# Performance work log

Measured on AMD Instinct MI355X. Metric: run time of the kernel, lower is better.

## Reference

```python
import jax, jax.numpy as jnp
import numpy as np

EPS = 1e-5


def _bn(x, g, b):
    # BatchNorm1d in training mode: batch mean, biased variance, eps=1e-5
    m = jnp.mean(x, axis=0)
    v = jnp.var(x, axis=0)
    return (x - m) * jax.lax.rsqrt(v + EPS) * g + b


def setup_inputs() -> dict:
    key = jax.random.key(0)
    ks = jax.random.split(key, 16)
    B, N, F, H = 4096, 128, 4, 32
    w = lambda k, o, i: jax.random.normal(k, (o, i), jnp.float32) * 0.3
    d = {
        'u': jax.random.normal(ks[0], (B, N, F), jnp.float32),
        'mask': jnp.ones((B * N, 1), jnp.int32),
        # MLPphi params
        'p_bn1_g': jnp.ones((F,), jnp.float32), 'p_bn1_b': jnp.zeros((F,), jnp.float32), 'p_w1': w(ks[1], H, F),
        'p_bn2_g': jnp.ones((H,), jnp.float32), 'p_bn2_b': jnp.zeros((H,), jnp.float32), 'p_w2': w(ks[2], H, H),
        'p_bn3_g': jnp.ones((H,), jnp.float32), 'p_bn3_b': jnp.zeros((H,), jnp.float32), 'p_w3': w(ks[3], H, H),
        # MLPomega params
        'o_bn1_g': jnp.ones((F,), jnp.float32), 'o_bn1_b': jnp.zeros((F,), jnp.float32), 'o_w1': w(ks[4], H, F),
        'o_bn2_g': jnp.ones((H,), jnp.float32), 'o_bn2_b': jnp.zeros((H,), jnp.float32), 'o_w2': w(ks[5], H, H),
        'o_bn3_g': jnp.ones((H,), jnp.float32), 'o_bn3_b': jnp.zeros((H,), jnp.float32), 'o_w3': w(ks[6], H, H),
        # MLPtheta params
        't_bn1_g': jnp.ones((H,), jnp.float32), 't_bn1_b': jnp.zeros((H,), jnp.float32), 't_w1': w(ks[7], H, H),
        't_bn2_g': jnp.ones((H,), jnp.float32), 't_bn2_b': jnp.zeros((H,), jnp.float32), 't_w2': w(ks[8], H, H),
        't_bn3_g': jnp.ones((H,), jnp.float32), 't_bn3_b': jnp.zeros((H,), jnp.float32), 't_w3': w(ks[9], H, H),
        't_bn4_g': jnp.ones((H,), jnp.float32), 't_bn4_b': jnp.zeros((H,), jnp.float32),
        't_w4': w(ks[10], 1, H), 't_b4': jnp.zeros((1,), jnp.float32),
    }
    return d


def _forward(u, mask,
             p_bn1_g, p_bn1_b, p_w1, p_bn2_g, p_bn2_b, p_w2, p_bn3_g, p_bn3_b, p_w3,
             o_bn1_g, o_bn1_b, o_w1, o_bn2_g, o_bn2_b, o_w2, o_bn3_g, o_bn3_b, o_w3,
             t_bn1_g, t_bn1_b, t_w1, t_bn2_g, t_bn2_b, t_w2, t_bn3_g, t_bn3_b, t_w3,
             t_bn4_g, t_bn4_b, t_w4, t_b4):
    B, N, F = u.shape
    H = p_w1.shape[0]
    u_flat = u.reshape(-1, F)  # (B*N, F)

    # MLPphi: three BN+Linear(no bias)+Tanh blocks with residual adds (dropout=identity in eval)
    o1 = jnp.tanh(_bn(u_flat, p_bn1_g, p_bn1_b) @ p_w1.T)
    o2 = jnp.tanh(_bn(o1, p_bn2_g, p_bn2_b) @ p_w2.T)
    o3 = jnp.tanh(_bn(o1 + o2, p_bn3_g, p_bn3_b) @ p_w3.T)
    x_main = (o1 + o2 + o3).reshape(B, N, H)

    # MLPomega: BN+Linear+Tanh x2, BN+Linear, softmax over hidden dim (dim=1 of flat), then masked_fill
    a = jnp.tanh(_bn(u_flat, o_bn1_g, o_bn1_b) @ o_w1.T)
    a = jnp.tanh(_bn(a, o_bn2_g, o_bn2_b) @ o_w2.T)
    a = _bn(a, o_bn3_g, o_bn3_b) @ o_w3.T
    a = jax.nn.softmax(a, axis=1)
    a = jnp.where(mask == 0, -jnp.inf, a)
    x_attn = a.reshape(B, N, H)

    # attention pooling over neighbors
    x = jnp.sum(x_main * x_attn, axis=1)  # (B, H)

    x = jnp.tanh(_bn(x, t_bn1_g, t_bn1_b) @ t_w1.T)
    x = jnp.tanh(_bn(x, t_bn2_g, t_bn2_b) @ t_w2.T)
    x = jnp.tanh(_bn(x, t_bn3_g, t_bn3_b) @ t_w3.T)
    x = _bn(x, t_bn4_g, t_bn4_b) @ t_w4.T + t_b4
    return x


def reference(u, mask,
              p_bn1_g, p_bn1_b, p_w1, p_bn2_g, p_bn2_b, p_w2, p_bn3_g, p_bn3_b, p_w3,
              o_bn1_g, o_bn1_b, o_w1, o_bn2_g, o_bn2_b, o_w2, o_bn3_g, o_bn3_b, o_w3,
              t_bn1_g, t_bn1_b, t_w1, t_bn2_g, t_bn2_b, t_w2, t_bn3_g, t_bn3_b, t_w3,
              t_bn4_g, t_bn4_b, t_w4, t_b4):
    return _forward(u, mask,
                    p_bn1_g, p_bn1_b, p_w1, p_bn2_g, p_bn2_b, p_w2, p_bn3_g, p_bn3_b, p_w3,
                    o_bn1_g, o_bn1_b, o_w1, o_bn2_g, o_bn2_b, o_w2, o_bn3_g, o_bn3_b, o_w3,
                    t_bn1_g, t_bn1_b, t_w1, t_bn2_g, t_bn2_b, t_w2, t_bn3_g, t_bn3_b, t_w3,
                    t_bn4_g, t_bn4_b, t_w4, t_b4)
```

## Files before the change

kernel.cpp:

```cpp
#include <hip/hip_runtime.h>

typedef unsigned int u32;
typedef unsigned short u16;
typedef __attribute__((ext_vector_type(8))) _Float16 half8;
typedef __attribute__((ext_vector_type(4))) float f32x4;

#define ROWS  524288
#define BROWS 4096
#define EPS   1e-5f

#define S_U   0
#define S_O1  8
#define S_A1  72
#define S_O12 136
#define S_A2  200
#define S_X   264
#define S_X1  328
#define S_X2  392
#define S_X3  456
#define SHARD 1024
#define NSH   64

#define XSTR 40

// ... 104 lines not shown
    float t = 0.f;
#pragma unroll
    for (int g=0; g<32; ++g) t += scr[tid + 8*g];
    mr[tid] = t;
  }
  __syncthreads();
  if (tid < 4){
    float s = mr[tid], q = mr[4+tid];
    float m = s*(1.0f/ROWS);
    float var = q*(1.0f/ROWS) - m*m;
    mr[tid]   = m;
    mr[4+tid] = rsqrtf(var + EPS);
  }
  __syncthreads();
}
template<bool F32>
__device__ __forceinline__ void bn_u_l(const float* mr, const void* g, const void* b,
                                       const float* f, float* xn){
#pragma unroll
  for (int k=0;k<4;++k)
    xn[k] = (f[k]-mr[k])*(rdp<F32>(g,k)*mr[4+k]) + rdp<F32>(b,k);
}

template<bool F32, bool STORE>
__device__ __forceinline__ void chain1_out(const float* xn, const void* W1, u16* Xrow,
                                           u16* __restrict__ grow){
  u32 buf[16];
#pragma unroll
  for (int jp=0; jp<16; ++jp){
    int j0 = 2*jp, j1 = 2*jp+1;
    float a0 = tanh_fast(xn[0]*rdp<F32>(W1,j0*4+0) + xn[1]*rdp<F32>(W1,j0*4+1)
                       + xn[2]*rdp<F32>(W1,j0*4+2) + xn[3]*rdp<F32>(W1,j0*4+3));
    float a1 = tanh_fast(xn[0]*rdp<F32>(W1,j1*4+0) + xn[1]*rdp<F32>(W1,j1*4+1)
                       + xn[2]*rdp<F32>(W1,j1*4+2) + xn[3]*rdp<F32>(W1,j1*4+3));
    buf[jp] = pack2h(a0, a1);
  }
#pragma unroll
  for (int c=0;c<4;++c){
    uint4 v; v.x = buf[c*4]; v.y = buf[c*4+1]; v.z = buf[c*4+2]; v.w = buf[c*4+3];
    *(uint4*)&Xrow[c*8] = v;
    if (STORE) *(uint4*)&grow[c*8] = v;
  }
}

template<bool F32>
__device__ __forceinline__ void fold2(const float* __restrict__ S, int offA, int offB,
    const void* gA, const void* bA, const void* WA,
    const void* gB, const void* bB, const void* WB,
    u16* Wt, float* Cb, float* scr )
{
  int tid = threadIdx.x;
  {
    int pair = tid >> 2;
    int isq  = (tid >> 1) & 1;
    int half = tid & 1;
    int L = pair >> 5, k = pair & 31;
    int off = (L ? offB : offA) + isq*32 + k;
    float t = 0.f;
#pragma unroll
    for (int i=0;i<32;++i)
      t += S[(half*32 + i)*SHARD + off];
    scr[tid] = t;
  }
  __syncthreads();
  if (tid < 64){
    int L = tid>>5, k = tid&31;
    const void* g = L? gB:gA; const void* b = L? bB:bA;
    float s = scr[tid*4+0] + scr[tid*4+1];
    float q = scr[tid*4+2] + scr[tid*4+3];
    float m    = s*(1.0f/ROWS);
    float var  = q*(1.0f/ROWS) - m*m;
    float rstd = rsqrtf(var+EPS);
    float sc = rdp<F32>(g,k)*rstd;
    scr[256+tid] = sc;
    scr[320+tid] = rdp<F32>(b,k) - m*sc;
  }
  __syncthreads();
  if (tid < 64){
    int L = tid>>5, j = tid&31;
    const void* W = L? WB:WA;
    float c = 0.f;
#pragma unroll
    for (int k=0;k<32;++k){
      float Wv = rdp<F32>(W, j*32+k);
      Wt[(L*32+j)*XSTR + k] = f2h(Wv * scr[256 + ((L<<5)|k)]);
      c += Wv * scr[320 + ((L<<5)|k)];
    }
    Cb[L*32+j] = c;
  }
  __syncthreads();
}

#define KIND_TANH          0
#define KIND_TANHRES       2
#define KIND_TANHRES_ATREG 3
template<int KIND>
__device__ __forceinline__ void mfma_layer(u16* X, const u16* Wt, const float* Cb,
                                           int L, int wv, int lane, const u32* at_pk)
{
  int ln15 = lane & 15, quad = lane >> 4;
  half8 w0 = *(const half8*)&Wt[(L*32 + ln15     )*XSTR + quad*8];
  half8 w1 = *(const half8*)&Wt[(L*32 + ln15 + 16)*XSTR + quad*8];
  float bias0[4], bias1[4];
#pragma unroll
  for (int reg=0;reg<4;++reg){
    bias0[reg] = Cb[L*32 +      quad*4 + reg];
    bias1[reg] = Cb[L*32 + 16 + quad*4 + reg];
// ... 102 lines not shown
    float s=0.f, q=0.f;
#pragma unroll
    for (int q2=0;q2<32;++q2){
      float v = Xs[(seg*32+q2)*33 + j];
      s += v; q = fmaf(v,v,q);
    }
    lds2[seg*32+j] = s;
    lds2[256 + seg*32+j] = q;
  }
  __syncthreads();
  if (tid < 64){
    int j = tid & 31; bool isq = tid >= 32;
    const float* src = lds2 + (isq?256:0);
    float tot=0.f;
#pragma unroll
    for (int sg=0;sg<8;++sg) tot += src[sg*32+j];
    atomicAdd(&S[shard*SHARD + offS + (isq?32:0) + j], tot);
  }
  __syncthreads();
}

template<bool F32, bool MAT>
__device__ __forceinline__ void pass1_body(const void* __restrict__ u,
    const void* pg1, const void* pb1, const void* pw1,
    const void* og1, const void* ob1, const void* ow1,
    float* __restrict__ S, u16* __restrict__ o1g, u16* __restrict__ a1g,
    u16* X, float* lds2, float* mr)
{
  int tid = threadIdx.x;
  int base = blockIdx.x*1024;
  int shard = blockIdx.x & (NSH-1);
  float f[4][4];
#pragma unroll
  for (int g=0; g<4; ++g) load_u4<F32>(u, base + g*256 + tid, f[g]);
  prep_u_par(S, mr, lds2, tid);

#pragma unroll
  for (int g=0; g<4; ++g){
    int r = base + g*256 + tid;
    float xn[4];
    bn_u_l<F32>(mr, pg1, pb1, f[g], xn);
    chain1_out<F32,MAT>(xn, pw1, X + tid*XSTR, o1g + (size_t)r*32);
    reduce_f16(X, lds2, S, S_O1, shard);

    bn_u_l<F32>(mr, og1, ob1, f[g], xn);
    chain1_out<F32,MAT>(xn, ow1, X + tid*XSTR, a1g + (size_t)r*32);
    reduce_f16(X, lds2, S, S_A1, shard);
  }
}
template<bool MAT>
__global__ __launch_bounds__(256) void k_pass1(const void* __restrict__ u,
    const void* pg1, const void* pb1, const void* pw1,
    const void* og1, const void* ob1, const void* ow1,
    float* __restrict__ S, u16* o1g, u16* a1g){
  __shared__ u16 X[256*XSTR];
  __shared__ float lds2[512];
  __shared__ float mr[8];
  __shared__ int sf;
  int isf = detect_u((const u16*)u, threadIdx.x, &sf);
  if (isf) pass1_body<true ,MAT>(u,pg1,pb1,pw1,og1,ob1,ow1,S,o1g,a1g,X,lds2,mr);
  else     pass1_body<false,MAT>(u,pg1,pb1,pw1,og1,ob1,ow1,S,o1g,a1g,X,lds2,mr);
}

#define P2_LOADM(BUF, G, MT) { \
  size_t R = (size_t)(gbase + (G)*256 + rowbase + (MT)*16 + ln15); \
  fo[BUF][MT] = *(const half8*)&o12g[R*32 + quad*8]; \
  fa[BUF][MT] = *(const half8*)&a2g [R*32 + quad*8]; }
#define P2_LOAD(BUF, G) P2_LOADM(BUF,G,0) P2_LOADM(BUF,G,1) P2_LOADM(BUF,G,2) P2_LOADM(BUF,G,3)

template<bool F32>
__device__ __forceinline__ void pass2m_body(
    const void* pg2, const void* pb2, const void* pw2,
    const void* og2, const void* ob2, const void* ow2,
    float* __restrict__ S, u16* __restrict__ o12g, u16* __restrict__ a2g,
    u16* Wt, float* Cb, float* lds2)
{
  int tid = threadIdx.x;
  int wv = tid >> 6, lane = tid & 63;
  int ln15 = lane & 15, quad = lane >> 4;
  int gbase = blockIdx.x*1024;
  int shard = blockIdx.x & (NSH-1);
  int rowbase = wv*64;

  half8 fo[2][4], fa[2][4];
  P2_LOAD(0, 0)

  fold2<F32>(S, S_O1, S_A1, pg2,pb2,pw2, og2,ob2,ow2, Wt, Cb, lds2);

  half8 w0o = *(const half8*)&Wt[(ln15     )*XSTR + quad*8];
  half8 w1o = *(const half8*)&Wt[(ln15 + 16)*XSTR + quad*8];
  half8 w0a = *(const half8*)&Wt[(32 + ln15     )*XSTR + quad*8];
  half8 w1a = *(const half8*)&Wt[(32 + ln15 + 16)*XSTR + quad*8];
  float b0o[4], b1o[4], b0a[4], b1a[4];
#pragma unroll
  for (int reg=0;reg<4;++reg){
    b0o[reg] = Cb[     quad*4 + reg]; b1o[reg] = Cb[16 + quad*4 + reg];
    b0a[reg] = Cb[32 + quad*4 + reg]; b1a[reg] = Cb[48 + quad*4 + reg];
  }

  float s8o[8], q8o[8], s8a[8], q8a[8];
#pragma unroll
  for (int i=0;i<8;++i){ s8o[i]=0.f; q8o[i]=0.f; s8a[i]=0.f; q8a[i]=0.f; }

#pragma unroll
  for (int g=0; g<4; ++g){
    const int buf = g & 1;
    if (g < 3){ P2_LOAD(buf^1, g+1) }
    uint2 r0[4], r1[4];
#pragma unroll
    for (int Mt=0; Mt<4; ++Mt){
      size_t R = (size_t)(gbase + g*256 + rowbase + Mt*16 + ln15);
      r0[Mt] = *(const uint2*)&o12g[R*32 +      quad*4];
      r1[Mt] = *(const uint2*)&o12g[R*32 + 16 + quad*4];
    }
#pragma unroll
    for (int Mt=0; Mt<4; ++Mt){
      size_t R = (size_t)(gbase + g*256 + rowbase + Mt*16 + ln15);
      {
        f32x4 c0 = {0.f,0.f,0.f,0.f}, c1 = {0.f,0.f,0.f,0.f};
        c0 = __builtin_amdgcn_mfma_f32_16x16x32_f16(w0o, fo[buf][Mt], c0, 0,0,0);
        c1 = __builtin_amdgcn_mfma_f32_16x16x32_f16(w1o, fo[buf][Mt], c1, 0,0,0);
        float o0[4], o1v[4];
        unpk4(r0[Mt], o0); unpk4(r1[Mt], o1v);
        float v0[4], v1[4];
#pragma unroll
        for (int reg=0;reg<4;++reg){
          float a = o0[reg]  + tanh_fast(c0[reg] + b0o[reg]);
          float b = o1v[reg] + tanh_fast(c1[reg] + b1o[reg]);
          s8o[reg]   += a; q8o[reg]   = fmaf(a,a,q8o[reg]);
          s8o[4+reg] += b; q8o[4+reg] = fmaf(b,b,q8o[4+reg]);
          v0[reg] = a; v1[reg] = b;
        }
        uint2 wA, wB;
        wA.x = pack2h(v0[0], v0[1]); wA.y = pack2h(v0[2], v0[3]);
        wB.x = pack2h(v1[0], v1[1]); wB.y = pack2h(v1[2], v1[3]);
        *(uint2*)&o12g[R*32 +      quad*4] = wA;
        *(uint2*)&o12g[R*32 + 16 + quad*4] = wB;
      }
      {
        f32x4 c0 = {0.f,0.f,0.f,0.f}, c1 = {0.f,0.f,0.f,0.f};
        c0 = __builtin_amdgcn_mfma_f32_16x16x32_f16(w0a, fa[buf][Mt], c0, 0,0,0);
        c1 = __builtin_amdgcn_mfma_f32_16x16x32_f16(w1a, fa[buf][Mt], c1, 0,0,0);
        float v0[4], v1[4];
#pragma unroll
        for (int reg=0;reg<4;++reg){
          float a = tanh_fast(c0[reg] + b0a[reg]);
          float b = tanh_fast(c1[reg] + b1a[reg]);
          s8a[reg]   += a; q8a[reg]   = fmaf(a,a,q8a[reg]);
          s8a[4+reg] += b; q8a[4+reg] = fmaf(b,b,q8a[4+reg]);
          v0[reg] = a; v1[reg] = b;
        }
        uint2 wA, wB;
        wA.x = pack2h(v0[0], v0[1]); wA.y = pack2h(v0[2], v0[3]);
        wB.x = pack2h(v1[0], v1[1]); wB.y = pack2h(v1[2], v1[3]);
        *(uint2*)&a2g[R*32 +      quad*4] = wA;
        *(uint2*)&a2g[R*32 + 16 + quad*4] = wB;
      }
    }
  }
  emit_stats(s8o, q8o, tid, wv, quad, ln15, lds2, S, S_O12, shard);
  emit_stats(s8a, q8a, tid, wv, quad, ln15, lds2, S, S_A2, shard);
}
__global__ __launch_bounds__(256) void k_pass2m(const void* __restrict__ u,
    const void* pg2, const void* pb2, const void* pw2,
    const void* og2, const void* ob2, const void* ow2,
    float* __restrict__ S, u16* o12g, u16* a2g){
  __shared__ u16 Wt[2*32*XSTR];
  __shared__ float Cb[64];
  __shared__ float lds2[512];
  __shared__ int sf;
  int isf = detect_u((const u16*)u, threadIdx.x, &sf);
  if (isf) pass2m_body<true >(pg2,pb2,pw2,og2,ob2,ow2,S,o12g,a2g,Wt,Cb,lds2);
  else     pass2m_body<false>(pg2,pb2,pw2,og2,ob2,ow2,S,o12g,a2g,Wt,Cb,lds2);
}

template<int KIND>
__device__ __forceinline__ void mfma_stat_l(const u16* X, const u16* Wt, const float* Cb,
    int L, int wv, int lane, float* s8, float* q8)
{
  int ln15 = lane & 15, quad = lane >> 4;
  half8 w0 = *(const half8*)&Wt[(L*32 + ln15     )*XSTR + quad*8];
  half8 w1 = *(const half8*)&Wt[(L*32 + ln15 + 16)*XSTR + quad*8];
  float bias0[4], bias1[4];
#pragma unroll
  for (int reg=0;reg<4;++reg){
    bias0[reg] = Cb[L*32 +      quad*4 + reg];
    bias1[reg] = Cb[L*32 + 16 + quad*4 + reg];
  }
#pragma unroll
  for (int i=0;i<8;++i){ s8[i]=0.f; q8[i]=0.f; }
  int rowbase = wv*64;
#pragma unroll
  for (int Mt=0; Mt<4; ++Mt){
    int s = rowbase + Mt*16 + ln15;
    half8 bfr = *(const half8*)&X[s*XSTR + quad*8];
    f32x4 c0 = {0.f,0.f,0.f,0.f}, c1 = {0.f,0.f,0.f,0.f};
// ... 43 lines not shown
  emit_stats(s8, q8, tid, wv, quad, ln15, lds2, S, S_O12, shard);

  bn_u_l<F32>(mr, og1, ob1, f, xn);
  chain1_out<F32,false>(xn, ow1, X + tid*XSTR, 0);
  __syncthreads();
  mfma_stat_l<KIND_TANH>(X, Wt, Cb, 1, wv, lane, s8, q8);
  emit_stats(s8, q8, tid, wv, quad, ln15, lds2, S, S_A2, shard);
}
__global__ __launch_bounds__(256) void k_pass2(const void* __restrict__ u,
    const void* pg1, const void* pb1, const void* pw1,
    const void* og1, const void* ob1, const void* ow1,
    const void* pg2, const void* pb2, const void* pw2,
    const void* og2, const void* ob2, const void* ow2,
    float* __restrict__ S){
  __shared__ u16 X[256*XSTR];
  __shared__ u16 Wt[2*32*XSTR];
  __shared__ float Cb[64];
  __shared__ float lds2[512];
  __shared__ float mr[8];
  __shared__ int sf;
  int isf = detect_u((const u16*)u, threadIdx.x, &sf);
  if (isf) pass2_body<true >(u,pg1,pb1,pw1,og1,ob1,ow1,pg2,pb2,pw2,og2,ob2,ow2,S,X,Wt,Cb,lds2,mr);
  else     pass2_body<false>(u,pg1,pb1,pw1,og1,ob1,ow1,pg2,pb2,pw2,og2,ob2,ow2,S,X,Wt,Cb,lds2,mr);
}

#define P3_LOADM(BUF, G, MT) { \
  size_t R = (size_t)(gbase + (G)*256 + rowbase + (MT)*16 + ln15); \
  fa[BUF][MT] = *(const half8*)&a2g [R*32 + quad*8]; \
  fo[BUF][MT] = *(const half8*)&o12g[R*32 + quad*8]; }
#define P3_LOAD(BUF, G) P3_LOADM(BUF,G,0) P3_LOADM(BUF,G,1) P3_LOADM(BUF,G,2) P3_LOADM(BUF,G,3)

template<bool F32>
__device__ __forceinline__ void pass3m_body(const int* __restrict__ mask,
    const void* pg3, const void* pb3, const void* pw3,
    const void* og3, const void* ob3, const void* ow3,
    const u16* __restrict__ o12g, const u16* __restrict__ a2g,
    float* __restrict__ x, float* __restrict__ S,
    u16* Wt, float* Cb, float* lds2)
{
  int tid = threadIdx.x;
  int wv = tid >> 6, lane = tid & 63;
  int ln15 = lane & 15, quad = lane >> 4;
  int gbase = blockIdx.x*1024;
  int shard = blockIdx.x & (NSH-1);
  int rowbase = wv*64;

  half8 fa[2][4], fo[2][4];
  P3_LOAD(0, 0)

  fold2<F32>(S, S_A2, S_O12, og3,ob3,ow3, pg3,pb3,pw3, Wt, Cb, lds2);

  half8 w0s = *(const half8*)&Wt[(ln15     )*XSTR + quad*8];
  half8 w1s = *(const half8*)&Wt[(ln15 + 16)*XSTR + quad*8];
  half8 w0p = *(const half8*)&Wt[(32 + ln15     )*XSTR + quad*8];
  half8 w1p = *(const half8*)&Wt[(32 + ln15 + 16)*XSTR + quad*8];
  float b0s[4], b1s[4], b0p[4], b1p[4];
#pragma unroll
  for (int reg=0;reg<4;++reg){
    b0s[reg] = Cb[     quad*4 + reg]; b1s[reg] = Cb[16 + quad*4 + reg];
    b0p[reg] = Cb[32 + quad*4 + reg]; b1p[reg] = Cb[48 + quad*4 + reg];
  }

#pragma unroll
  for (int g=0; g<4; ++g){
    const int buf = g & 1;
    if (g < 3){ P3_LOAD(buf^1, g+1) }
    uint2 r0[4], r1[4];
#pragma unroll
    for (int Mt=0; Mt<4; ++Mt){
      size_t R = (size_t)(gbase + g*256 + rowbase + Mt*16 + ln15);
      r0[Mt] = *(const uint2*)&o12g[R*32 +      quad*4];
      r1[Mt] = *(const uint2*)&o12g[R*32 + 16 + quad*4];
    }
    int maskbase = gbase + g*256 + wv*64;
    u32 at_pk[16];
#pragma unroll
    for (int Mt=0; Mt<4; ++Mt){
      f32x4 c0 = {0.f,0.f,0.f,0.f}, c1 = {0.f,0.f,0.f,0.f};
      c0 = __builtin_amdgcn_mfma_f32_16x16x32_f16(w0s, fa[buf][Mt], c0, 0,0,0);
      c1 = __builtin_amdgcn_mfma_f32_16x16x32_f16(w1s, fa[buf][Mt], c1, 0,0,0);
      float l0[4], l1[4];
#pragma unroll
      for (int reg=0;reg<4;++reg){ l0[reg] = c0[reg]+b0s[reg]; l1[reg] = c1[reg]+b1s[reg]; }
      float mx = l0[0];
#pragma unroll
      for (int reg=1;reg<4;++reg) mx = fmaxf(mx, l0[reg]);
#pragma unroll
      for (int reg=0;reg<4;++reg) mx = fmaxf(mx, l1[reg]);
      mx = fmaxf(mx, __shfl_xor(mx, 16));
      mx = fmaxf(mx, __shfl_xor(mx, 32));
      float sum = 0.f;
#pragma unroll
      for (int reg=0;reg<4;++reg){ l0[reg] = __expf(l0[reg]-mx); sum += l0[reg]; }
#pragma unroll
      for (int reg=0;reg<4;++reg){ l1[reg] = __expf(l1[reg]-mx); sum += l1[reg]; }
      sum += __shfl_xor(sum, 16);
      sum += __shfl_xor(sum, 32);
      float inv = __builtin_amdgcn_rcpf(sum);
      bool mz = (mask[maskbase + Mt*16 + ln15] == 0);
#pragma unroll
      for (int reg=0;reg<4;++reg){
        l0[reg] *= inv; l1[reg] *= inv;
        if (mz){ l0[reg] = -__builtin_inff(); l1[reg] = -__builtin_inff(); }
      }
      at_pk[Mt*4+0] = pack2h(l0[0], l0[1]);
      at_pk[Mt*4+1] = pack2h(l0[2], l0[3]);
      at_pk[Mt*4+2] = pack2h(l1[0], l1[1]);
      at_pk[Mt*4+3] = pack2h(l1[2], l1[3]);
    }
    float ps[8];
#pragma unroll
    for (int i=0;i<8;++i) ps[i]=0.f;
#pragma unroll
    for (int Mt=0; Mt<4; ++Mt){
      f32x4 c0 = {0.f,0.f,0.f,0.f}, c1 = {0.f,0.f,0.f,0.f};
      c0 = __builtin_amdgcn_mfma_f32_16x16x32_f16(w0p, fo[buf][Mt], c0, 0,0,0);
      c1 = __builtin_amdgcn_mfma_f32_16x16x32_f16(w1p, fo[buf][Mt], c1, 0,0,0);
      float o0[4], o1v[4];
      unpk4(r0[Mt], o0); unpk4(r1[Mt], o1v);
      float a0v[4], a1v[4];
      a0v[0]=lo16(at_pk[Mt*4+0]); a0v[1]=hi16(at_pk[Mt*4+0]);
      a0v[2]=lo16(at_pk[Mt*4+1]); a0v[3]=hi16(at_pk[Mt*4+1]);
      a1v[0]=lo16(at_pk[Mt*4+2]); a1v[1]=hi16(at_pk[Mt*4+2]);
      a1v[2]=lo16(at_pk[Mt*4+3]); a1v[3]=hi16(at_pk[Mt*4+3]);
#pragma unroll
      for (int reg=0;reg<4;++reg){
        float a = (o0[reg]  + tanh_fast(c0[reg]+b0p[reg])) * a0v[reg];
        float b = (o1v[reg] + tanh_fast(c1[reg]+b1p[reg])) * a1v[reg];
        ps[reg]   += a;
        ps[4+reg] += b;
      }
    }
#pragma unroll
    for (int i=0;i<8;++i) ps[i]=red16(ps[i]);
    __syncthreads();
    if (ln15 == 0){
#pragma unroll
      for (int rg=0; rg<4; ++rg){
        lds2[wv*32 + quad*4+rg]    = ps[rg];
        lds2[wv*32 + 16+quad*4+rg] = ps[4+rg];
      }
    }
    __syncthreads();
    if (tid < 64){
      int half = tid >> 5, j = tid & 31;
      float v = lds2[half*64 + j] + lds2[half*64 + 32 + j];
      x[((size_t)blockIdx.x*8 + g*2 + half)*32 + j] = v;
      float* Sh = S + shard*SHARD;
      atomicAdd(&Sh[S_X+j], v);
      atomicAdd(&Sh[S_X+32+j], v*v);
    }
  }
}
__global__ __launch_bounds__(256) void k_pass3m(const void* __restrict__ u, const int* __restrict__ mask,
    const void* pg3, const void* pb3, const void* pw3,
    const void* og3, const void* ob3, const void* ow3,
    const u16* o12g, const u16* a2g,
    float* __restrict__ x, float* __restrict__ S){
  __shared__ u16 Wt[2*32*XSTR];
  __shared__ float Cb[64];
  __shared__ float lds2[512];
  __shared__ int sf;
  int isf = detect_u((const u16*)u, threadIdx.x, &sf);
  if (isf) pass3m_body<true >(mask,pg3,pb3,pw3,og3,ob3,ow3,o12g,a2g,x,S,Wt,Cb,lds2);
  else     pass3m_body<false>(mask,pg3,pb3,pw3,og3,ob3,ow3,o12g,a2g,x,S,Wt,Cb,lds2);
}

template<bool F32>
__device__ __forceinline__ void fold4(const float* __restrict__ S,
    int off0,int off1,int off2,int off3,
    const void* g0,const void* b0,const void* W0,
    const void* g1,const void* b1,const void* W1,
    const void* g2,const void* b2,const void* W2,
    const void* g3,const void* b3,const void* W3,
    u16* Wt, float* Cb, float* scr)
{
  int tid = threadIdx.x;
  __shared__ float scr2[256];
  if (tid < 128){
    int L = tid>>5, k = tid&31;
    const void* g = (L==0)?g0:(L==1)?g1:(L==2)?g2:g3;
    const void* b = (L==0)?b0:(L==1)?b1:(L==2)?b2:b3;
    int off = (L==0)?off0:(L==1)?off1:(L==2)?off2:off3;
    float s=0.f, q=0.f;
#pragma unroll
    for (int sh=0; sh<NSH; ++sh){
      s += S[sh*SHARD + off + k];
      q += S[sh*SHARD + off + 32 + k];
// ... 260 lines not shown
}

extern "C" void kernel_launch(void* const* d_in, const int* in_sizes, int n_in,
                              void* d_out, int out_size, void* d_ws, size_t ws_size,
                              hipStream_t stream)
{
  const void* u    = d_in[0];
  const int*  mask = (const int*)d_in[1];
  const void *pg1=d_in[2],  *pb1=d_in[3],  *pw1=d_in[4];
  const void *pg2=d_in[5],  *pb2=d_in[6],  *pw2=d_in[7];
  const void *pg3=d_in[8],  *pb3=d_in[9],  *pw3=d_in[10];
  const void *og1=d_in[11], *ob1=d_in[12], *ow1=d_in[13];
  const void *og2=d_in[14], *ob2=d_in[15], *ow2=d_in[16];
  const void *og3=d_in[17], *ob3=d_in[18], *ow3=d_in[19];
  const void *tg1=d_in[20], *tb1=d_in[21], *tw1=d_in[22];
  const void *tg2=d_in[23], *tb2=d_in[24], *tw2=d_in[25];
  const void *tg3=d_in[26], *tb3=d_in[27], *tw3=d_in[28];
  const void *tg4=d_in[29], *tb4=d_in[30], *tw4=d_in[31], *tbb4=d_in[32];

  char* ws = (char*)d_ws;
  float* S    = (float*)(ws + 4096);
  float* x    = (float*)(ws + 524288);
  float* xb   = (float*)(ws + 1048576);

  const size_t MB = 1024*1024;
  u16* o12g = (u16*)(ws + 8*MB);
  u16* a2g  = (u16*)(ws + 40*MB);
  bool MAT = ws_size >= 73*MB;

  (void)hipMemsetAsync(ws, 0, 4096 + NSH*SHARD*4, stream);
  k_stats_u<<<1024, 256, 0, stream>>>(u, S);
  if (MAT){
    k_pass1<true ><<<512, 256, 0, stream>>>(u, pg1,pb1,pw1, og1,ob1,ow1, S, o12g, a2g);
    k_pass2m<<<512, 256, 0, stream>>>(u, pg2,pb2,pw2, og2,ob2,ow2, S, o12g, a2g);
    k_pass3m<<<512, 256, 0, stream>>>(u, mask, pg3,pb3,pw3, og3,ob3,ow3, o12g, a2g, x, S);
  } else {
    k_pass1<false><<<512, 256, 0, stream>>>(u, pg1,pb1,pw1, og1,ob1,ow1, S, o12g, a2g);
    k_pass2<<<2048, 256, 0, stream>>>(u, pg1,pb1,pw1, og1,ob1,ow1,
                                      pg2,pb2,pw2, og2,ob2,ow2, S);
    k_pass3<<<2048, 256, 0, stream>>>(u, mask, pg1,pb1,pw1, og1,ob1,ow1,
                                      pg2,pb2,pw2, og2,ob2,ow2,
                                      pg3,pb3,pw3, og3,ob3,ow3, x, S);
  }
  k_theta_L<64><<<16, 256, 0, stream>>>(u, x,  xb, S, S_X,  S_X1, tg1, tb1, tw1);
  k_theta_L<16><<<16, 256, 0, stream>>>(u, xb, x,  S, S_X1, S_X2, tg2, tb2, tw2);
  k_theta_L<16><<<16, 256, 0, stream>>>(u, x,  xb, S, S_X2, S_X3, tg3, tb3, tw3);
  k_theta_fin<<<16, 256, 0, stream>>>(u, xb, S, tg4, tb4, tw4, tbb4, d_out);
}
```

Measured before the change: 308.7 us.

## Hoist BN-weight folding into single-block kernels and simplify pass kernels

```diff
diff --git a/kernel.cpp b/kernel.cpp
--- a/kernel.cpp
+++ b/kernel.cpp
@@ -150,32 +150,48 @@
     xn[k] = (f[k]-mr[k])*(rdp<F32>(g,k)*mr[4+k]) + rdp<F32>(b,k);
 }
 
-template<bool F32, bool STORE>
-__device__ __forceinline__ void chain1_out(const float* xn, const void* W1, u16* Xrow,
-                                           u16* __restrict__ grow){
-  u32 buf[16];
-#pragma unroll
-  for (int jp=0; jp<16; ++jp){
-    int j0 = 2*jp, j1 = 2*jp+1;
-    float a0 = tanh_fast(xn[0]*rdp<F32>(W1,j0*4+0) + xn[1]*rdp<F32>(W1,j0*4+1)
-                       + xn[2]*rdp<F32>(W1,j0*4+2) + xn[3]*rdp<F32>(W1,j0*4+3));
-    float a1 = tanh_fast(xn[0]*rdp<F32>(W1,j1*4+0) + xn[1]*rdp<F32>(W1,j1*4+1)
-                       + xn[2]*rdp<F32>(W1,j1*4+2) + xn[3]*rdp<F32>(W1,j1*4+3));
-    buf[jp] = pack2h(a0, a1);
-  }
-#pragma unroll
-  for (int c=0;c<4;++c){
-    uint4 v; v.x = buf[c*4]; v.y = buf[c*4+1]; v.z = buf[c*4+2]; v.w = buf[c*4+3];
-    *(uint4*)&Xrow[c*8] = v;
-    if (STORE) *(uint4*)&grow[c*8] = v;
-  }
-}
-
 template<bool F32>
-__device__ __forceinline__ void fold2(const float* __restrict__ S, int offA, int offB,
-    const void* gA, const void* bA, const void* WA,
-    const void* gB, const void* bB, const void* WB,
-    u16* Wt, float* Cb, float* scr )
+__device__ __forceinline__ void fold1_body(
+    const void* pg1,const void* pb1,const void* pw1,
+    const void* og1,const void* ob1,const void* ow1,
+    const float* __restrict__ S, float* __restrict__ F1, float* scr, float* mr)
+{
+  int tid = threadIdx.x;
+  prep_u_par(S, mr, scr, tid);
+  if (tid < 64){
+    int side = tid>>5, jj = tid&31;
+    const void* W = side? ow1:pw1;
+    const void* g = side? og1:pg1;
+    const void* b = side? ob1:pb1;
+    float c = 0.f;
+#pragma unroll
+    for (int k=0;k<4;++k){
+      float sc = rdp<F32>(g,k)*mr[4+k];
+      float sh = rdp<F32>(b,k) - mr[k]*sc;
+      float wv = rdp<F32>(W, jj*4+k);
+      F1[side*128 + jj*4 + k] = wv*sc;
+      c += wv*sh;
+    }
+    F1[256 + side*32 + jj] = c;
+  }
+}
+__global__ __launch_bounds__(256) void k_fold1(const void* __restrict__ u,
+    const void* pg1,const void* pb1,const void* pw1,
+    const void* og1,const void* ob1,const void* ow1,
+    const float* __restrict__ S, float* __restrict__ F1){
+  __shared__ float scr[256];
+  __shared__ float mr[8];
+  __shared__ int sf;
+  int isf = detect_u((const u16*)u, threadIdx.x, &sf);
+  if (isf) fold1_body<true >(pg1,pb1,pw1,og1,ob1,ow1,S,F1,scr,mr);
+  else     fold1_body<false>(pg1,pb1,pw1,og1,ob1,ow1,S,F1,scr,mr);
+}
+
+template<bool F32>
+__device__ __forceinline__ void foldw_body(const float* __restrict__ S, int offA, int offB,
+    const void* gA,const void* bA,const void* WA,
+    const void* gB,const void* bB,const void* WB,
+    u16* __restrict__ WTg, float* __restrict__ CBg, float* scr)
 {
   int tid = threadIdx.x;
   {
@@ -211,6 +227,107 @@
 #pragma unroll
     for (int k=0;k<32;++k){
       float Wv = rdp<F32>(W, j*32+k);
+      WTg[(L*32+j)*32 + k] = f2h(Wv * scr[256 + ((L<<5)|k)]);
+      c += Wv * scr[320 + ((L<<5)|k)];
+    }
+    CBg[L*32+j] = c;
+  }
+}
+__global__ __launch_bounds__(256) void k_foldw(const void* __restrict__ u,
+    const float* __restrict__ S, int offA, int offB,
+    const void* gA,const void* bA,const void* WA,
+    const void* gB,const void* bB,const void* WB,
+    u16* __restrict__ WTg, float* __restrict__ CBg){
+  __shared__ float scr[512];
+  __shared__ int sf;
+  int isf = detect_u((const u16*)u, threadIdx.x, &sf);
+  if (isf) foldw_body<true >(S,offA,offB,gA,bA,WA,gB,bB,WB,WTg,CBg,scr);
+  else     foldw_body<false>(S,offA,offB,gA,bA,WA,gB,bB,WB,WTg,CBg,scr);
+}
+
+template<bool STORE>
+__device__ __forceinline__ void chain1f(const float* f, const float* __restrict__ Wf,
+                                        const float* __restrict__ cf,
+                                        u16* Xrow, u16* __restrict__ grow){
+  u32 buf[16];
+#pragma unroll
+  for (int jp=0; jp<16; ++jp){
+    int j0 = 2*jp, j1 = 2*jp+1;
+    float a0 = tanh_fast(fmaf(f[0],Wf[j0*4+0], fmaf(f[1],Wf[j0*4+1],
+                         fmaf(f[2],Wf[j0*4+2], fmaf(f[3],Wf[j0*4+3], cf[j0])))));
+    float a1 = tanh_fast(fmaf(f[0],Wf[j1*4+0], fmaf(f[1],Wf[j1*4+1],
+                         fmaf(f[2],Wf[j1*4+2], fmaf(f[3],Wf[j1*4+3], cf[j1])))));
+    buf[jp] = pack2h(a0, a1);
+  }
+#pragma unroll
+  for (int c=0;c<4;++c){
+    uint4 v; v.x = buf[c*4]; v.y = buf[c*4+1]; v.z = buf[c*4+2]; v.w = buf[c*4+3];
+    *(uint4*)&Xrow[c*8] = v;
+    if (STORE) *(uint4*)&grow[c*8] = v;
+  }
+}
+
+template<bool F32, bool STORE>
+__device__ __forceinline__ void chain1_out(const float* xn, const void* W1, u16* Xrow,
+                                           u16* __restrict__ grow){
+  u32 buf[16];
+#pragma unroll
+  for (int jp=0; jp<16; ++jp){
+    int j0 = 2*jp, j1 = 2*jp+1;
+    float a0 = tanh_fast(xn[0]*rdp<F32>(W1,j0*4+0) + xn[1]*rdp<F32>(W1,j0*4+1)
+                       + xn[2]*rdp<F32>(W1,j0*4+2) + xn[3]*rdp<F32>(W1,j0*4+3));
+    float a1 = tanh_fast(xn[0]*rdp<F32>(W1,j1*4+0) + xn[1]*rdp<F32>(W1,j1*4+1)
+                       + xn[2]*rdp<F32>(W1,j1*4+2) + xn[3]*rdp<F32>(W1,j1*4+3));
+    buf[jp] = pack2h(a0, a1);
+  }
+#pragma unroll
+  for (int c=0;c<4;++c){
+    uint4 v; v.x = buf[c*4]; v.y = buf[c*4+1]; v.z = buf[c*4+2]; v.w = buf[c*4+3];
+    *(uint4*)&Xrow[c*8] = v;
+    if (STORE) *(uint4*)&grow[c*8] = v;
+  }
+}
+
+template<bool F32>
+__device__ __forceinline__ void fold2(const float* __restrict__ S, int offA, int offB,
+    const void* gA, const void* bA, const void* WA,
+    const void* gB, const void* bB, const void* WB,
+    u16* Wt, float* Cb, float* scr )
+{
+  int tid = threadIdx.x;
+  {
+    int pair = tid >> 2;
+    int isq  = (tid >> 1) & 1;
+    int half = tid & 1;
+    int L = pair >> 5, k = pair & 31;
+    int off = (L ? offB : offA) + isq*32 + k;
+    float t = 0.f;
+#pragma unroll
+    for (int i=0;i<32;++i)
+      t += S[(half*32 + i)*SHARD + off];
+    scr[tid] = t;
+  }
+  __syncthreads();
+  if (tid < 64){
+    int L = tid>>5, k = tid&31;
+    const void* g = L? gB:gA; const void* b = L? bB:bA;
+    float s = scr[tid*4+0] + scr[tid*4+1];
+    float q = scr[tid*4+2] + scr[tid*4+3];
+    float m    = s*(1.0f/ROWS);
+    float var  = q*(1.0f/ROWS) - m*m;
+    float rstd = rsqrtf(var+EPS);
+    float sc = rdp<F32>(g,k)*rstd;
+    scr[256+tid] = sc;
+    scr[320+tid] = rdp<F32>(b,k) - m*sc;
+  }
+  __syncthreads();
+  if (tid < 64){
+    int L = tid>>5, j = tid&31;
+    const void* W = L? WB:WA;
+    float c = 0.f;
+#pragma unroll
+    for (int k=0;k<32;++k){
+      float Wv = rdp<F32>(W, j*32+k);
       Wt[(L*32+j)*XSTR + k] = f2h(Wv * scr[256 + ((L<<5)|k)]);
       c += Wv * scr[320 + ((L<<5)|k)];
     }
@@ -359,59 +476,82 @@
 
 template<bool F32, bool MAT>
 __device__ __forceinline__ void pass1_body(const void* __restrict__ u,
-    const void* pg1, const void* pb1, const void* pw1,
-    const void* og1, const void* ob1, const void* ow1,
-    float* __restrict__ S, u16* __restrict__ o1g, u16* __restrict__ a1g,
-    u16* X, float* lds2, float* mr)
+    const float* __restrict__ F1, float* __restrict__ S,
+    u16* __restrict__ o1g, u16* __restrict__ a1g,
+    u16* X, float* lds2)
 {
   int tid = threadIdx.x;
   int base = blockIdx.x*1024;
   int shard = blockIdx.x & (NSH-1);
+  const float* W1p = F1;
+  const float* W1o = F1 + 128;
+  const float* c1p = F1 + 256;
+  const float* c1o = F1 + 288;
   float f[4][4];
 #pragma unroll
   for (int g=0; g<4; ++g) load_u4<F32>(u, base + g*256 + tid, f[g]);
-  prep_u_par(S, mr, lds2, tid);
+
+  int j = tid & 31, seg = tid >> 5;
+  float sa0=0.f, qa0=0.f, sa1=0.f, qa1=0.f;
 
 #pragma unroll
   for (int g=0; g<4; ++g){
     int r = base + g*256 + tid;
-    float xn[4];
-    bn_u_l<F32>(mr, pg1, pb1, f[g], xn);
-    chain1_out<F32,MAT>(xn, pw1, X + tid*XSTR, o1g + (size_t)r*32);
-    reduce_f16(X, lds2, S, S_O1, shard);
-
-    bn_u_l<F32>(mr, og1, ob1, f[g], xn);
-    chain1_out<F32,MAT>(xn, ow1, X + tid*XSTR, a1g + (size_t)r*32);
-    reduce_f16(X, lds2, S, S_A1, shard);
+    chain1f<MAT>(f[g], W1p, c1p, X + tid*XSTR, o1g + (size_t)r*32);
+    __syncthreads();
+#pragma unroll
+    for (int q2=0;q2<32;++q2){
+      float v = h2f(X[(seg*32+q2)*XSTR + j]);
+      sa0 += v; qa0 = fmaf(v,v,qa0);
+    }
+    __syncthreads();
+    chain1f<MAT>(f[g], W1o, c1o, X + tid*XSTR, a1g + (size_t)r*32);
+    __syncthreads();
+#pragma unroll
+    for (int q2=0;q2<32;++q2){
+      float v = h2f(X[(seg*32+q2)*XSTR + j]);
+      sa1 += v; qa1 = fmaf(v,v,qa1);
+    }
+    __syncthreads();
+  }
+  lds2[tid] = sa0; lds2[256+tid] = qa0;
+  __syncthreads();
+  if (tid < 64){
+    int j2 = tid & 31; bool isq = tid >= 32;
+    const float* src = lds2 + (isq?256:0);
+    float tot=0.f;
+#pragma unroll
+    for (int sg=0;sg<8;++sg) tot += src[sg*32+j2];
+    atomicAdd(&S[shard*SHARD + S_O1 + (isq?32:0) + j2], tot);
+  }
+  __syncthreads();
+  lds2[tid] = sa1; lds2[256+tid] = qa1;
+  __syncthreads();
+  if (tid < 64){
+    int j2 = tid & 31; bool isq = tid >= 32;
+    const float* src = lds2 + (isq?256:0);
+    float tot=0.f;
+#pragma unroll
+    for (int sg=0;sg<8;++sg) tot += src[sg*32+j2];
+    atomicAdd(&S[shard*SHARD + S_A1 + (isq?32:0) + j2], tot);
   }
 }
 template<bool MAT>
 __global__ __launch_bounds__(256) void k_pass1(const void* __restrict__ u,
-    const void* pg1, const void* pb1, const void* pw1,
-    const void* og1, const void* ob1, const void* ow1,
-    float* __restrict__ S, u16* o1g, u16* a1g){
+    const float* __restrict__ F1, float* __restrict__ S, u16* o1g, u16* a1g){
   __shared__ u16 X[256*XSTR];
   __shared__ float lds2[512];
-  __shared__ float mr[8];
   __shared__ int sf;
   int isf = detect_u((const u16*)u, threadIdx.x, &sf);
-  if (isf) pass1_body<true ,MAT>(u,pg1,pb1,pw1,og1,ob1,ow1,S,o1g,a1g,X,lds2,mr);
-  else     pass1_body<false,MAT>(u,pg1,pb1,pw1,og1,ob1,ow1,S,o1g,a1g,X,lds2,mr);
-}
-
-#define P2_LOADM(BUF, G, MT) { \
-  size_t R = (size_t)(gbase + (G)*256 + rowbase + (MT)*16 + ln15); \
-  fo[BUF][MT] = *(const half8*)&o12g[R*32 + quad*8]; \
-  fa[BUF][MT] = *(const half8*)&a2g [R*32 + quad*8]; }
-#define P2_LOAD(BUF, G) P2_LOADM(BUF,G,0) P2_LOADM(BUF,G,1) P2_LOADM(BUF,G,2) P2_LOADM(BUF,G,3)
-
-template<bool F32>
-__device__ __forceinline__ void pass2m_body(
-    const void* pg2, const void* pb2, const void* pw2,
-    const void* og2, const void* ob2, const void* ow2,
-    float* __restrict__ S, u16* __restrict__ o12g, u16* __restrict__ a2g,
-    u16* Wt, float* Cb, float* lds2)
-{
+  if (isf) pass1_body<true ,MAT>(u,F1,S,o1g,a1g,X,lds2);
+  else     pass1_body<false,MAT>(u,F1,S,o1g,a1g,X,lds2);
+}
+
+__global__ __launch_bounds__(256, 3) void k_pass2m(
+    const u16* __restrict__ WT, const float* __restrict__ CB,
+    float* __restrict__ S, u16* __restrict__ o12g, u16* __restrict__ a2g)
+{
+  __shared__ float lds2[512];
   int tid = threadIdx.x;
   int wv = tid >> 6, lane = tid & 63;
   int ln15 = lane & 15, quad = lane >> 4;
@@ -419,20 +559,15 @@
   int shard = blockIdx.x & (NSH-1);
   int rowbase = wv*64;
 
-  half8 fo[2][4], fa[2][4];
-  P2_LOAD(0, 0)
-
-  fold2<F32>(S, S_O1, S_A1, pg2,pb2,pw2, og2,ob2,ow2, Wt, Cb, lds2);
-
-  half8 w0o = *(const half8*)&Wt[(ln15     )*XSTR + quad*8];
-  half8 w1o = *(const half8*)&Wt[(ln15 + 16)*XSTR + quad*8];
-  half8 w0a = *(const half8*)&Wt[(32 + ln15     )*XSTR + quad*8];
-  half8 w1a = *(const half8*)&Wt[(32 + ln15 + 16)*XSTR + quad*8];
+  half8 w0o = *(const half8*)&WT[(ln15     )*32 + quad*8];
+  half8 w1o = *(const half8*)&WT[(ln15 + 16)*32 + quad*8];
+  half8 w0a = *(const half8*)&WT[(32 + ln15     )*32 + quad*8];
+  half8 w1a = *(const half8*)&WT[(32 + ln15 + 16)*32 + quad*8];
   float b0o[4], b1o[4], b0a[4], b1a[4];
 #pragma unroll
   for (int reg=0;reg<4;++reg){
-    b0o[reg] = Cb[     quad*4 + reg]; b1o[reg] = Cb[16 + quad*4 + reg];
-    b0a[reg] = Cb[32 + quad*4 + reg]; b1a[reg] = Cb[48 + quad*4 + reg];
+    b0o[reg] = CB[     quad*4 + reg]; b1o[reg] = CB[16 + quad*4 + reg];
+    b0a[reg] = CB[32 + quad*4 + reg]; b1a[reg] = CB[48 + quad*4 + reg];
   }
 
   float s8o[8], q8o[8], s8a[8], q8a[8];
@@ -441,12 +576,12 @@
 
 #pragma unroll
   for (int g=0; g<4; ++g){
-    const int buf = g & 1;
-    if (g < 3){ P2_LOAD(buf^1, g+1) }
-    uint2 r0[4], r1[4];
+    half8 fo[4], fa[4]; uint2 r0[4], r1[4];
 #pragma unroll
     for (int Mt=0; Mt<4; ++Mt){
       size_t R = (size_t)(gbase + g*256 + rowbase + Mt*16 + ln15);
+      fo[Mt] = *(const half8*)&o12g[R*32 + quad*8];
+      fa[Mt] = *(const half8*)&a2g [R*32 + quad*8];
       r0[Mt] = *(const uint2*)&o12g[R*32 +      quad*4];
       r1[Mt] = *(const uint2*)&o12g[R*32 + 16 + quad*4];
     }
@@ -455,8 +590,8 @@
       size_t R = (size_t)(gbase + g*256 + rowbase + Mt*16 + ln15);
       {
         f32x4 c0 = {0.f,0.f,0.f,0.f}, c1 = {0.f,0.f,0.f,0.f};
-        c0 = __builtin_amdgcn_mfma_f32_16x16x32_f16(w0o, fo[buf][Mt], c0, 0,0,0);
-        c1 = __builtin_amdgcn_mfma_f32_16x16x32_f16(w1o, fo[buf][Mt], c1, 0,0,0);
+        c0 = __builtin_amdgcn_mfma_f32_16x16x32_f16(w0o, fo[Mt], c0, 0,0,0);
+        c1 = __builtin_amdgcn_mfma_f32_16x16x32_f16(w1o, fo[Mt], c1, 0,0,0);
         float o0[4], o1v[4];
         unpk4(r0[Mt], o0); unpk4(r1[Mt], o1v);
         float v0[4], v1[4];
@@ -476,8 +611,8 @@
       }
       {
         f32x4 c0 = {0.f,0.f,0.f,0.f}, c1 = {0.f,0.f,0.f,0.f};
-        c0 = __builtin_amdgcn_mfma_f32_16x16x32_f16(w0a, fa[buf][Mt], c0, 0,0,0);
-        c1 = __builtin_amdgcn_mfma_f32_16x16x32_f16(w1a, fa[buf][Mt], c1, 0,0,0);
+        c0 = __builtin_amdgcn_mfma_f32_16x16x32_f16(w0a, fa[Mt], c0, 0,0,0);
+        c1 = __builtin_amdgcn_mfma_f32_16x16x32_f16(w1a, fa[Mt], c1, 0,0,0);
         float v0[4], v1[4];
 #pragma unroll
         for (int reg=0;reg<4;++reg){
@@ -498,17 +633,121 @@
   emit_stats(s8o, q8o, tid, wv, quad, ln15, lds2, S, S_O12, shard);
   emit_stats(s8a, q8a, tid, wv, quad, ln15, lds2, S, S_A2, shard);
 }
-__global__ __launch_bounds__(256) void k_pass2m(const void* __restrict__ u,
-    const void* pg2, const void* pb2, const void* pw2,
-    const void* og2, const void* ob2, const void* ow2,
-    float* __restrict__ S, u16* o12g, u16* a2g){
-  __shared__ u16 Wt[2*32*XSTR];
-  __shared__ float Cb[64];
+
+__global__ __launch_bounds__(256, 3) void k_pass3m(const int* __restrict__ mask,
+    const u16* __restrict__ WT, const float* __restrict__ CB,
+    const u16* __restrict__ o12g, const u16* __restrict__ a2g,
+    float* __restrict__ x, float* __restrict__ S)
+{
   __shared__ float lds2[512];
-  __shared__ int sf;
-  int isf = detect_u((const u16*)u, threadIdx.x, &sf);
-  if (isf) pass2m_body<true >(pg2,pb2,pw2,og2,ob2,ow2,S,o12g,a2g,Wt,Cb,lds2);
-  else     pass2m_body<false>(pg2,pb2,pw2,og2,ob2,ow2,S,o12g,a2g,Wt,Cb,lds2);
+  int tid = threadIdx.x;
+  int wv = tid >> 6, lane = tid & 63;
+  int ln15 = lane & 15, quad = lane >> 4;
+  int gbase = blockIdx.x*1024;
+  int shard = blockIdx.x & (NSH-1);
+  int rowbase = wv*64;
+
+  half8 w0s = *(const half8*)&WT[(ln15     )*32 + quad*8];
+  half8 w1s = *(const half8*)&WT[(ln15 + 16)*32 + quad*8];
+  half8 w0p = *(const half8*)&WT[(32 + ln15     )*32 + quad*8];
+  half8 w1p = *(const half8*)&WT[(32 + ln15 + 16)*32 + quad*8];
+  float b0s[4], b1s[4], b0p[4], b1p[4];
+#pragma unroll
+  for (int reg=0;reg<4;++reg){
+    b0s[reg] = CB[     quad*4 + reg]; b1s[reg] = CB[16 + quad*4 + reg];
+    b0p[reg] = CB[32 + quad*4 + reg]; b1p[reg] = CB[48 + quad*4 + reg];
+  }
+
+#pragma unroll
+  for (int g=0; g<4; ++g){
+    half8 fa[4], fo[4]; uint2 r0[4], r1[4];
+#pragma unroll
+    for (int Mt=0; Mt<4; ++Mt){
+      size_t R = (size_t)(gbase + g*256 + rowbase + Mt*16 + ln15);
+      fa[Mt] = *(const half8*)&a2g [R*32 + quad*8];
+      fo[Mt] = *(const half8*)&o12g[R*32 + quad*8];
+      r0[Mt] = *(const uint2*)&o12g[R*32 +      quad*4];
+      r1[Mt] = *(const uint2*)&o12g[R*32 + 16 + quad*4];
+    }
+    int maskbase = gbase + g*256 + wv*64;
+    u32 at_pk[16];
+#pragma unroll
+    for (int Mt=0; Mt<4; ++Mt){
+      f32x4 c0 = {0.f,0.f,0.f,0.f}, c1 = {0.f,0.f,0.f,0.f};
+      c0 = __builtin_amdgcn_mfma_f32_16x16x32_f16(w0s, fa[Mt], c0, 0,0,0);
+      c1 = __builtin_amdgcn_mfma_f32_16x16x32_f16(w1s, fa[Mt], c1, 0,0,0);
+      float l0[4], l1[4];
+#pragma unroll
+      for (int reg=0;reg<4;++reg){ l0[reg] = c0[reg]+b0s[reg]; l1[reg] = c1[reg]+b1s[reg]; }
+      float mx = l0[0];
+#pragma unroll
+      for (int reg=1;reg<4;++reg) mx = fmaxf(mx, l0[reg]);
+#pragma unroll
+      for (int reg=0;reg<4;++reg) mx = fmaxf(mx, l1[reg]);
+      mx = fmaxf(mx, __shfl_xor(mx, 16));
+      mx = fmaxf(mx, __shfl_xor(mx, 32));
+      float sum = 0.f;
+#pragma unroll
+      for (int reg=0;reg<4;++reg){ l0[reg] = __expf(l0[reg]-mx); sum += l0[reg]; }
+#pragma unroll
+      for (int reg=0;reg<4;++reg){ l1[reg] = __expf(l1[reg]-mx); sum += l1[reg]; }
+      sum += __shfl_xor(sum, 16);
+      sum += __shfl_xor(sum, 32);
+      float inv = __builtin_amdgcn_rcpf(sum);
+      bool mz = (mask[maskbase + Mt*16 + ln15] == 0);
+#pragma unroll
+      for (int reg=0;reg<4;++reg){
+        l0[reg] *= inv; l1[reg] *= inv;
+        if (mz){ l0[reg] = -__builtin_inff(); l1[reg] = -__builtin_inff(); }
+      }
+      at_pk[Mt*4+0] = pack2h(l0[0], l0[1]);
+      at_pk[Mt*4+1] = pack2h(l0[2], l0[3]);
+      at_pk[Mt*4+2] = pack2h(l1[0], l1[1]);
+      at_pk[Mt*4+3] = pack2h(l1[2], l1[3]);
+    }
+    float ps[8];
+#pragma unroll
+    for (int i=0;i<8;++i) ps[i]=0.f;
+#pragma unroll
+    for (int Mt=0; Mt<4; ++Mt){
+      f32x4 c0 = {0.f,0.f,0.f,0.f}, c1 = {0.f,0.f,0.f,0.f};
+      c0 = __builtin_amdgcn_mfma_f32_16x16x32_f16(w0p, fo[Mt], c0, 0,0,0);
+      c1 = __builtin_amdgcn_mfma_f32_16x16x32_f16(w1p, fo[Mt], c1, 0,0,0);
+      float o0[4], o1v[4];
+      unpk4(r0[Mt], o0); unpk4(r1[Mt], o1v);
+      float a0v[4], a1v[4];
+      a0v[0]=lo16(at_pk[Mt*4+0]); a0v[1]=hi16(at_pk[Mt*4+0]);
+      a0v[2]=lo16(at_pk[Mt*4+1]); a0v[3]=hi16(at_pk[Mt*4+1]);
+      a1v[0]=lo16(at_pk[Mt*4+2]); a1v[1]=hi16(at_pk[Mt*4+2]);
+      a1v[2]=lo16(at_pk[Mt*4+3]); a1v[3]=hi16(at_pk[Mt*4+3]);
+#pragma unroll
+      for (int reg=0;reg<4;++reg){
+        float a = (o0[reg]  + tanh_fast(c0[reg]+b0p[reg])) * a0v[reg];
+        float b = (o1v[reg] + tanh_fast(c1[reg]+b1p[reg])) * a1v[reg];
+        ps[reg]   += a;
+        ps[4+reg] += b;
+      }
+    }
+#pragma unroll
+    for (int i=0;i<8;++i) ps[i]=red16(ps[i]);
+    __syncthreads();
+    if (ln15 == 0){
+#pragma unroll
+      for (int rg=0; rg<4; ++rg){
+        lds2[wv*32 + quad*4+rg]    = ps[rg];
+        lds2[wv*32 + 16+quad*4+rg] = ps[4+rg];
+      }
+    }
+    __syncthreads();
+    if (tid < 64){
+      int half = tid >> 5, j = tid & 31;
+      float v = lds2[half*64 + j] + lds2[half*64 + 32 + j];
+      x[((size_t)blockIdx.x*8 + g*2 + half)*32 + j] = v;
+      float* Sh = S + shard*SHARD;
+      atomicAdd(&Sh[S_X+j], v);
+      atomicAdd(&Sh[S_X+32+j], v*v);
+    }
+  }
 }
 
 template<int KIND>
@@ -598,148 +837,6 @@
   int isf = detect_u((const u16*)u, threadIdx.x, &sf);
   if (isf) pass2_body<true >(u,pg1,pb1,pw1,og1,ob1,ow1,pg2,pb2,pw2,og2,ob2,ow2,S,X,Wt,Cb,lds2,mr);
   else     pass2_body<false>(u,pg1,pb1,pw1,og1,ob1,ow1,pg2,pb2,pw2,og2,ob2,ow2,S,X,Wt,Cb,lds2,mr);
-}
-
-#define P3_LOADM(BUF, G, MT) { \
-  size_t R = (size_t)(gbase + (G)*256 + rowbase + (MT)*16 + ln15); \
-  fa[BUF][MT] = *(const half8*)&a2g [R*32 + quad*8]; \
-  fo[BUF][MT] = *(const half8*)&o12g[R*32 + quad*8]; }
-#define P3_LOAD(BUF, G) P3_LOADM(BUF,G,0) P3_LOADM(BUF,G,1) P3_LOADM(BUF,G,2) P3_LOADM(BUF,G,3)
-
-template<bool F32>
-__device__ __forceinline__ void pass3m_body(const int* __restrict__ mask,
-    const void* pg3, const void* pb3, const void* pw3,
-    const void* og3, const void* ob3, const void* ow3,
-    const u16* __restrict__ o12g, const u16* __restrict__ a2g,
-    float* __restrict__ x, float* __restrict__ S,
-    u16* Wt, float* Cb, float* lds2)
-{
-  int tid = threadIdx.x;
-  int wv = tid >> 6, lane = tid & 63;
-  int ln15 = lane & 15, quad = lane >> 4;
-  int gbase = blockIdx.x*1024;
-  int shard = blockIdx.x & (NSH-1);
-  int rowbase = wv*64;
-
-  half8 fa[2][4], fo[2][4];
-  P3_LOAD(0, 0)
-
-  fold2<F32>(S, S_A2, S_O12, og3,ob3,ow3, pg3,pb3,pw3, Wt, Cb, lds2);
-
-  half8 w0s = *(const half8*)&Wt[(ln15     )*XSTR + quad*8];
-  half8 w1s = *(const half8*)&Wt[(ln15 + 16)*XSTR + quad*8];
-  half8 w0p = *(const half8*)&Wt[(32 + ln15     )*XSTR + quad*8];
-  half8 w1p = *(const half8*)&Wt[(32 + ln15 + 16)*XSTR + quad*8];
-  float b0s[4], b1s[4], b0p[4], b1p[4];
-#pragma unroll
-  for (int reg=0;reg<4;++reg){
-    b0s[reg] = Cb[     quad*4 + reg]; b1s[reg] = Cb[16 + quad*4 + reg];
-    b0p[reg] = Cb[32 + quad*4 + reg]; b1p[reg] = Cb[48 + quad*4 + reg];
-  }
-
-#pragma unroll
-  for (int g=0; g<4; ++g){
-    const int buf = g & 1;
-    if (g < 3){ P3_LOAD(buf^1, g+1) }
-    uint2 r0[4], r1[4];
-#pragma unroll
-    for (int Mt=0; Mt<4; ++Mt){
-      size_t R = (size_t)(gbase + g*256 + rowbase + Mt*16 + ln15);
-      r0[Mt] = *(const uint2*)&o12g[R*32 +      quad*4];
-      r1[Mt] = *(const uint2*)&o12g[R*32 + 16 + quad*4];
-    }
-    int maskbase = gbase + g*256 + wv*64;
-    u32 at_pk[16];
-#pragma unroll
-    for (int Mt=0; Mt<4; ++Mt){
-      f32x4 c0 = {0.f,0.f,0.f,0.f}, c1 = {0.f,0.f,0.f,0.f};
-      c0 = __builtin_amdgcn_mfma_f32_16x16x32_f16(w0s, fa[buf][Mt], c0, 0,0,0);
-      c1 = __builtin_amdgcn_mfma_f32_16x16x32_f16(w1s, fa[buf][Mt], c1, 0,0,0);
-      float l0[4], l1[4];
-#pragma unroll
-      for (int reg=0;reg<4;++reg){ l0[reg] = c0[reg]+b0s[reg]; l1[reg] = c1[reg]+b1s[reg]; }
-      float mx = l0[0];
-#pragma unroll
-      for (int reg=1;reg<4;++reg) mx = fmaxf(mx, l0[reg]);
-#pragma unroll
-      for (int reg=0;reg<4;++reg) mx = fmaxf(mx, l1[reg]);
-      mx = fmaxf(mx, __shfl_xor(mx, 16));
-      mx = fmaxf(mx, __shfl_xor(mx, 32));
-      float sum = 0.f;
-#pragma unroll
-      for (int reg=0;reg<4;++reg){ l0[reg] = __expf(l0[reg]-mx); sum += l0[reg]; }
-#pragma unroll
-      for (int reg=0;reg<4;++reg){ l1[reg] = __expf(l1[reg]-mx); sum += l1[reg]; }
-      sum += __shfl_xor(sum, 16);
-      sum += __shfl_xor(sum, 32);
-      float inv = __builtin_amdgcn_rcpf(sum);
-      bool mz = (mask[maskbase + Mt*16 + ln15] == 0);
-#pragma unroll
-      for (int reg=0;reg<4;++reg){
-        l0[reg] *= inv; l1[reg] *= inv;
-        if (mz){ l0[reg] = -__builtin_inff(); l1[reg] = -__builtin_inff(); }
-      }
-      at_pk[Mt*4+0] = pack2h(l0[0], l0[1]);
-      at_pk[Mt*4+1] = pack2h(l0[2], l0[3]);
-      at_pk[Mt*4+2] = pack2h(l1[0], l1[1]);
-      at_pk[Mt*4+3] = pack2h(l1[2], l1[3]);
-    }
-    float ps[8];
-#pragma unroll
-    for (int i=0;i<8;++i) ps[i]=0.f;
-#pragma unroll
-    for (int Mt=0; Mt<4; ++Mt){
-      f32x4 c0 = {0.f,0.f,0.f,0.f}, c1 = {0.f,0.f,0.f,0.f};
-      c0 = __builtin_amdgcn_mfma_f32_16x16x32_f16(w0p, fo[buf][Mt], c0, 0,0,0);
-      c1 = __builtin_amdgcn_mfma_f32_16x16x32_f16(w1p, fo[buf][Mt], c1, 0,0,0);
-      float o0[4], o1v[4];
-      unpk4(r0[Mt], o0); unpk4(r1[Mt], o1v);
-      float a0v[4], a1v[4];
-      a0v[0]=lo16(at_pk[Mt*4+0]); a0v[1]=hi16(at_pk[Mt*4+0]);
-      a0v[2]=lo16(at_pk[Mt*4+1]); a0v[3]=hi16(at_pk[Mt*4+1]);
-      a1v[0]=lo16(at_pk[Mt*4+2]); a1v[1]=hi16(at_pk[Mt*4+2]);
-      a1v[2]=lo16(at_pk[Mt*4+3]); a1v[3]=hi16(at_pk[Mt*4+3]);
-#pragma unroll
-      for (int reg=0;reg<4;++reg){
-        float a = (o0[reg]  + tanh_fast(c0[reg]+b0p[reg])) * a0v[reg];
-        float b = (o1v[reg] + tanh_fast(c1[reg]+b1p[reg])) * a1v[reg];
-        ps[reg]   += a;
-        ps[4+reg] += b;
-      }
-    }
-#pragma unroll
-    for (int i=0;i<8;++i) ps[i]=red16(ps[i]);
-    __syncthreads();
-    if (ln15 == 0){
-#pragma unroll
-      for (int rg=0; rg<4; ++rg){
-        lds2[wv*32 + quad*4+rg]    = ps[rg];
-        lds2[wv*32 + 16+quad*4+rg] = ps[4+rg];
-      }
-    }
-    __syncthreads();
-    if (tid < 64){
-      int half = tid >> 5, j = tid & 31;
-      float v = lds2[half*64 + j] + lds2[half*64 + 32 + j];
-      x[((size_t)blockIdx.x*8 + g*2 + half)*32 + j] = v;
-      float* Sh = S + shard*SHARD;
-      atomicAdd(&Sh[S_X+j], v);
-      atomicAdd(&Sh[S_X+32+j], v*v);
-    }
-  }
-}
-__global__ __launch_bounds__(256) void k_pass3m(const void* __restrict__ u, const int* __restrict__ mask,
-    const void* pg3, const void* pb3, const void* pw3,
-    const void* og3, const void* ob3, const void* ow3,
-    const u16* o12g, const u16* a2g,
-    float* __restrict__ x, float* __restrict__ S){
-  __shared__ u16 Wt[2*32*XSTR];
-  __shared__ float Cb[64];
-  __shared__ float lds2[512];
-  __shared__ int sf;
-  int isf = detect_u((const u16*)u, threadIdx.x, &sf);
-  if (isf) pass3m_body<true >(mask,pg3,pb3,pw3,og3,ob3,ow3,o12g,a2g,x,S,Wt,Cb,lds2);
-  else     pass3m_body<false>(mask,pg3,pb3,pw3,og3,ob3,ow3,o12g,a2g,x,S,Wt,Cb,lds2);
 }
 
 template<bool F32>
@@ -1046,6 +1143,11 @@
   float* S    = (float*)(ws + 4096);
   float* x    = (float*)(ws + 524288);
   float* xb   = (float*)(ws + 1048576);
+  float* F1   = (float*)(ws + 1572864);
+  u16*   WT2  = (u16*)  (ws + 1572864 + 4096);
+  float* CB2  = (float*)(ws + 1572864 + 8192);
+  u16*   WT3  = (u16*)  (ws + 1572864 + 12288);
+  float* CB3  = (float*)(ws + 1572864 + 16384);
 
   const size_t MB = 1024*1024;
   u16* o12g = (u16*)(ws + 8*MB);
@@ -1054,12 +1156,15 @@
 
   (void)hipMemsetAsync(ws, 0, 4096 + NSH*SHARD*4, stream);
   k_stats_u<<<1024, 256, 0, stream>>>(u, S);
+  k_fold1<<<1, 256, 0, stream>>>(u, pg1,pb1,pw1, og1,ob1,ow1, S, F1);
   if (MAT){
-    k_pass1<true ><<<512, 256, 0, stream>>>(u, pg1,pb1,pw1, og1,ob1,ow1, S, o12g, a2g);
-    k_pass2m<<<512, 256, 0, stream>>>(u, pg2,pb2,pw2, og2,ob2,ow2, S, o12g, a2g);
-    k_pass3m<<<512, 256, 0, stream>>>(u, mask, pg3,pb3,pw3, og3,ob3,ow3, o12g, a2g, x, S);
+    k_pass1<true ><<<512, 256, 0, stream>>>(u, F1, S, o12g, a2g);
+    k_foldw<<<1, 256, 0, stream>>>(u, S, S_O1, S_A1, pg2,pb2,pw2, og2,ob2,ow2, WT2, CB2);
+    k_pass2m<<<512, 256, 0, stream>>>(WT2, CB2, S, o12g, a2g);
+    k_foldw<<<1, 256, 0, stream>>>(u, S, S_A2, S_O12, og3,ob3,ow3, pg3,pb3,pw3, WT3, CB3);
+    k_pass3m<<<512, 256, 0, stream>>>(mask, WT3, CB3, o12g, a2g, x, S);
   } else {
-    k_pass1<false><<<512, 256, 0, stream>>>(u, pg1,pb1,pw1, og1,ob1,ow1, S, o12g, a2g);
+    k_pass1<false><<<512, 256, 0, stream>>>(u, F1, S, o12g, a2g);
     k_pass2<<<2048, 256, 0, stream>>>(u, pg1,pb1,pw1, og1,ob1,ow1,
                                       pg2,pb2,pw2, og2,ob2,ow2, S);
     k_pass3<<<2048, 256, 0, stream>>>(u, mask, pg1,pb1,pw1, og1,ob1,ow1,
```

Result: slower. 496.0 us (+60.7%).
